# Kernel tuning notes

Hardware: AMD Instinct MI355X
Metric: run time of the kernel (lower is better)

The kernel has to match this reference:

```python
import jax, jax.numpy as jnp
import numpy as np

EPS = 1e-7  # keras backend epsilon
B, D_IN, H, L, DEPTH = 16384, 784, 512, 32, 2

def _lrelu(x):
    return jax.nn.leaky_relu(x, 0.3)  # tf.keras LeakyReLU default alpha

def _router(h, W1, b1, W2, b2, W3, b3):
    h = _lrelu(h @ W1 + b1)
    h = _lrelu(h @ W2 + b2)
    return jax.nn.sigmoid((h @ W3 + b3)[:, 0])

def setup_inputs():
    key = jax.random.key(0)
    ks = jax.random.split(key, 20)
    s = 0.02
    n = lambda k, sh: jax.random.normal(k, sh, jnp.float32) * s
    return {
        'x': jax.random.uniform(ks[0], (B, D_IN), jnp.float32),
        'enc_W0': n(ks[1], (D_IN, H)), 'enc_b0': jnp.zeros((H,), jnp.float32),
        'enc_W': n(ks[2], (3, H, H)), 'enc_b': jnp.zeros((3, H), jnp.float32),
        'dense_Wmu': n(ks[3], (7, H, L)), 'dense_bmu': jnp.zeros((7, L), jnp.float32),
        'dense_Wsig': n(ks[4], (7, H, L)), 'dense_bsig': jnp.zeros((7, L), jnp.float32),
        'trans_Wh': n(ks[5], (6, L, H)), 'trans_bh': jnp.zeros((6, H), jnp.float32),
        'trans_Wmu': n(ks[6], (6, H, L)), 'trans_bmu': jnp.zeros((6, L), jnp.float32),
        'trans_Wsig': n(ks[7], (6, H, L)), 'trans_bsig': jnp.zeros((6, L), jnp.float32),
        'routp_W1': n(ks[8], (3, L, H)), 'routp_b1': jnp.zeros((3, H), jnp.float32),
        'routp_W2': n(ks[9], (3, H, H)), 'routp_b2': jnp.zeros((3, H), jnp.float32),
        'routp_W3': n(ks[10], (3, H, 1)), 'routp_b3': jnp.zeros((3, 1), jnp.float32),
        'routq_W1': n(ks[11], (3, H, H)), 'routq_b1': jnp.zeros((3, H), jnp.float32),
        'routq_W2': n(ks[12], (3, H, H)), 'routq_b2': jnp.zeros((3, H), jnp.float32),
        'routq_W3': n(ks[13], (3, H, 1)), 'routq_b3': jnp.zeros((3, 1), jnp.float32),
        'dec_W1': n(ks[14], (4, L, H)), 'dec_b1': jnp.zeros((4, H), jnp.float32),
        'dec_W2': n(ks[15], (4, H, D_IN)), 'dec_b2': jnp.zeros((4, D_IN), jnp.float32),
    }

def reference(x, enc_W0, enc_b0, enc_W, enc_b,
              dense_Wmu, dense_bmu, dense_Wsig, dense_bsig,
              trans_Wh, trans_bh, trans_Wmu, trans_bmu, trans_Wsig, trans_bsig,
              routp_W1, routp_b1, routp_W2, routp_b2, routp_W3, routp_b3,
              routq_W1, routq_b1, routq_W2, routq_b2, routq_W3, routq_b3,
              dec_W1, dec_b1, dec_W2, dec_b2):
    Bn = x.shape[0]
    # bottom-up encoder chain; encoders collects layers i >= len - (depth+1) = 1
    d = _lrelu(x @ enc_W0 + enc_b0)
    encoders = []
    for i in range(3):
        d = _lrelu(d @ enc_W[i] + enc_b[i])
        encoders.append(d)
    depth_of = [0, 1, 1, 2, 2, 2, 2]  # BFS depth of the 7 tree nodes
    probs = {0: jnp.ones((Bn,), x.dtype)}
    zs = {}
    kl_nodes_tot = jnp.zeros((Bn,), x.dtype)
    kl_dec_tot = jnp.zeros((Bn,), x.dtype)
    kl_root = None
    leaves_prob, recons = [], []
    base = jax.random.key(1)
    for k in range(7):
        dl = depth_of[k]
        d = encoders[DEPTH - dl]
        mu_q_hat = d @ dense_Wmu[k] + dense_bmu[k]
        sig_q_hat = jax.nn.softplus(d @ dense_Wsig[k] + dense_bsig[k])
        if k == 0:
            mu_p = jnp.zeros_like(mu_q_hat)
            sig_p = jnp.ones_like(sig_q_hat)
            mu_q, sig_q = mu_q_hat, sig_q_hat
        else:
            zp = zs[(k - 1) // 2]
            h = _lrelu(zp @ trans_Wh[k - 1] + trans_bh[k - 1])
            mu_p = h @ trans_Wmu[k - 1] + trans_bmu[k - 1]
            sig_p = jax.nn.softplus(h @ trans_Wsig[k - 1] + trans_bsig[k - 1])
            # compute_posterior: precision-weighted fusion
            sig_q = 1.0 / (1.0 / sig_q_hat + 1.0 / sig_p)
            mu_q = sig_q * (mu_q_hat / sig_q_hat + mu_p / sig_p)
        vq = sig_q + EPS
        vp = sig_p + EPS
        # KL(N(mu_q, vq) || N(mu_p, vp)) for diag Gaussians (scale = sqrt(sigma+eps))
        kl = 0.5 * jnp.sum(vq / vp + (mu_q - mu_p) ** 2 / vp - 1.0 + jnp.log(vp / vq), axis=1)
        kl_node = jnp.clip(probs[k] * kl, -1.0, 1000.0)
        if k == 0:
            kl_root = kl_node
        else:
            kl_nodes_tot = kl_nodes_tot + kl_node
        eps_n = jax.random.normal(jax.random.fold_in(base, k), mu_q.shape, x.dtype)
        z = mu_q + jnp.sqrt(vq) * eps_n  # reparameterized sample
        zs[k] = z
        if k < 3:  # internal node: routing
            pl = _router(z, routp_W1[k], routp_b1[k], routp_W2[k], routp_b2[k], routp_W3[k], routp_b3[k])
            plq = _router(d, routq_W1[k], routq_b1[k], routq_W2[k], routq_b2[k], routq_W3[k], routq_b3[k])
            kl_dec = plq * jnp.log(EPS + plq / (pl + EPS)) + (1.0 - plq) * jnp.log(EPS + (1.0 - plq) / (1.0 - pl + EPS))
            kl_dec_tot = kl_dec_tot + probs[k] * kl_dec
            probs[2 * k + 1] = probs[k] * plq
            probs[2 * k + 2] = probs[k] * (1.0 - plq)
        else:  # leaf: decode
            leaves_prob.append(probs[k])
            h = _lrelu(z @ dec_W1[k - 3] + dec_b1[k - 3])
            recons.append(jax.nn.sigmoid(h @ dec_W2[k - 3] + dec_b2[k - 3]))
    rec_losses = jnp.zeros((Bn,), x.dtype)
    for p, r in zip(leaves_prob, recons):
        bce = -jnp.sum(x * jnp.log(r + EPS) + (1.0 - x) * jnp.log(1.0 - r + EPS), axis=1)
        rec_losses = rec_losses + p * bce
    # elbo_samples, per-sample total loss (shape [B])
    return kl_nodes_tot + kl_dec_tot + kl_root + rec_losses
```

## Files before the change

### kernel.cpp

```cpp
#include <hip/hip_runtime.h>
#include <cstdint>
#include <cstddef>

#define B_ROWS 16384
#define DIN 784
#define HD 512
#define LD 32
#define BMT 64

typedef __attribute__((ext_vector_type(8))) short short8;
typedef __attribute__((ext_vector_type(4))) float f32x4;
typedef __attribute__((ext_vector_type(4))) unsigned short us4;

struct I4 { int x, y, z, w; };
__device__ inline int i4get(I4 v, int z) { return z == 0 ? v.x : z == 1 ? v.y : z == 2 ? v.z : v.w; }

__device__ inline unsigned short f2bf(float v) {
  union { float f; unsigned u; } x; x.f = v;
  unsigned r = x.u + 0x7fffu + ((x.u >> 16) & 1u);
  return (unsigned short)(r >> 16);
}
__device__ inline float bf2f(unsigned short b) {
  union { unsigned u; float f; } x; x.u = ((unsigned)b) << 16;
  return x.f;
}

__host__ __device__ inline void threefry2x32(uint32_t k0, uint32_t k1,
                                             uint32_t x0, uint32_t x1,
                                             uint32_t& o0, uint32_t& o1) {
  uint32_t ks2 = k0 ^ k1 ^ 0x1BD11BDAu;
#define TF_ROT(x, d) (((x) << (d)) | ((x) >> (32 - (d))))
#define TF_R(r) { x0 += x1; x1 = TF_ROT(x1, r); x1 ^= x0; }
  x0 += k0; x1 += k1;
  TF_R(13) TF_R(15) TF_R(26) TF_R(6)
  x0 += k1; x1 += ks2 + 1u;
  TF_R(17) TF_R(29) TF_R(16) TF_R(24)
  x0 += ks2; x1 += k0 + 2u;
  TF_R(13) TF_R(15) TF_R(26) TF_R(6)
  x0 += k0; x1 += k1 + 3u;
  TF_R(17) TF_R(29) TF_R(16) TF_R(24)
  x0 += k1; x1 += ks2 + 4u;
  TF_R(13) TF_R(15) TF_R(26) TF_R(6)
  x0 += ks2; x1 += k0 + 5u;
  o0 = x0; o1 = x1;
#undef TF_R
#undef TF_ROT
}

__device__ inline float erfinv_f(float x) {
  float w = -log1pf(-x * x);
  float p;
  if (w < 5.0f) {
    w -= 2.5f;
    p = 2.81022636e-08f;
    p = fmaf(p, w, 3.43273939e-07f);
    p = fmaf(p, w, -3.5233877e-06f);
    p = fmaf(p, w, -4.39150654e-06f);
    p = fmaf(p, w, 0.00021858087f);
    p = fmaf(p, w, -0.00125372503f);
    p = fmaf(p, w, -0.00417768164f);
    p = fmaf(p, w, 0.246640727f);
    p = fmaf(p, w, 1.50140941f);
  } else {
    w = sqrtf(w) - 3.0f;
    p = -0.000200214257f;
    p = fmaf(p, w, 0.000100950558f);
    p = fmaf(p, w, 0.00134934322f);
    p = fmaf(p, w, -0.00367342844f);
    p = fmaf(p, w, 0.00573950773f);
    p = fmaf(p, w, -0.0076224613f);
    p = fmaf(p, w, 0.00943887047f);
    p = fmaf(p, w, 1.00167406f);
    p = fmaf(p, w, 2.83297682f);
  }
  return p * x;
}

__device__ inline float jax_normal_elem(uint32_t ka, uint32_t kb, uint32_t idx) {
  uint32_t b1, b2;
  threefry2x32(ka, kb, 0u, idx, b1, b2);
  uint32_t bits = b1 ^ b2;
  uint32_t fb = (bits >> 9) | 0x3f800000u;
  float f = __uint_as_float(fb) - 1.0f;
  const float lo = -0.99999994f;
  float u = f * 2.0f + lo;
  u = fmaxf(u, lo);
  return 1.41421356f * erfinv_f(u);
}

struct WJob {
  unsigned short pi;
  unsigned src_off, dst_off, start;
  short K, N, Np, Kp;
};
struct WJobs { WJob j[56]; unsigned total; };

constexpr WJobs make_jobs() {
  WJobs W{};
  int idx = 0; unsigned start = 0; unsigned d = 0;
  auto add = [&](int pi, unsigned so, int K, int N, int Np, int Kp, unsigned doff) {
    W.j[idx].pi = (unsigned short)pi; W.j[idx].src_off = so; W.j[idx].dst_off = doff;
    W.j[idx].start = start; W.j[idx].K = (short)K; W.j[idx].N = (short)N;
    W.j[idx].Np = (short)Np; W.j[idx].Kp = (short)Kp;
    start += (unsigned)(Np * Kp); ++idx;
  };
  add(0, 0, 784, 512, 512, 832, d); d += 512 * 832;
  for (int i = 0; i < 3; ++i) { add(1, i * 262144u, 512, 512, 512, 512, d); d += 262144; }
  for (int k = 0; k < 7; ++k) { add(2, k * 16384u, 512, 32, 32, 512, d);
                                add(3, k * 16384u, 512, 32, 32, 512, d + 16384); d += 32768; }
  for (int i = 0; i < 6; ++i) { add(4, i * 16384u, 32, 512, 512, 32, d); d += 16384; }
  for (int i = 0; i < 6; ++i) { add(5, i * 16384u, 512, 32, 32, 512, d);
                                add(6, i * 16384u, 512, 32, 32, 512, d + 16384); d += 32768; }
  for (int k = 0; k < 3; ++k) { add(7, k * 16384u, 32, 512, 512, 32, d); d += 16384; }
  for (int k = 0; k < 3; ++k) { add(8, k * 262144u, 512, 512, 512, 512, d); d += 262144; }
  for (int k = 0; k < 3; ++k) { add(9, k * 262144u, 512, 512, 512, 512, d); d += 262144; }
  for (int k = 0; k < 3; ++k) { add(10, k * 262144u, 512, 512, 512, 512, d); d += 262144; }
  for (int i = 0; i < 4; ++i) { add(11, i * 16384u, 32, 512, 512, 32, d); d += 16384; }
  for (int i = 0; i < 4; ++i) { add(12, i * 401408u, 512, 784, 896, 512, d); d += 458752; }
  W.total = start;
  return W;
}
__device__ constexpr WJobs g_jobs = make_jobs();

struct TileTable { unsigned ts[57]; };
constexpr TileTable make_tiles() {
  TileTable T{}; WJobs J = make_jobs();
  unsigned acc = 0;
  for (int i = 0; i < 56; ++i) {
    T.ts[i] = acc;
    acc += (unsigned)(J.j[i].Np / 32) * (unsigned)(J.j[i].Kp / 32);
  }
  T.ts[56] = acc;
  return T;
}
__device__ constexpr TileTable g_tiles = make_tiles();

#define OFF_ENC0T 0u
#define OFF_ENCT 425984u
#define OFF_DENSE 1212416u
#define OFF_TWH 1441792u
#define OFF_TMS 1540096u
#define OFF_RP1 1736704u
#define OFF_RP2 1785856u
#define OFF_RQ1 2572288u
#define OFF_RQ2 3358720u
#define OFF_DC1 4145152u
#define OFF_DC2 4210688u
#define ARENA_ELEMS 6045696u

struct WSrcs { const float* p[13]; };

__global__ void wconv_k(WSrcs srcs, unsigned short* __restrict__ arena) {
  __shared__ unsigned short tile[32][34];
  unsigned bid = blockIdx.x;
  int jo = 0;
#pragma unroll 1
  while (jo + 1 < 56 && g_tiles.ts[jo + 1] <= bid) ++jo;
  const WJob J = g_jobs.j[jo];
  unsigned t = bid - g_tiles.ts[jo];
  unsigned ktiles = (unsigned)J.Kp / 32u;
  unsigned n0 = (t / ktiles) * 32u, k0 = (t % ktiles) * 32u;
  int ty = threadIdx.x >> 3, tx4 = (threadIdx.x & 7) * 4;
  float v0 = 0, v1 = 0, v2 = 0, v3 = 0;
  int kk = (int)k0 + ty;
  if (kk < J.K) {
    const float* sp = srcs.p[J.pi] + J.src_off + (size_t)kk * J.N + n0 + tx4;
    int nb = (int)(n0 + tx4);
    if (nb + 3 < J.N) {
      float4 v = *reinterpret_cast<const float4*>(sp);
      v0 = v.x; v1 = v.y; v2 = v.z; v3 = v.w;
    } else {
      if (nb + 0 < J.N) v0 = sp[0];
      if (nb + 1 < J.N) v1 = sp[1];
      if (nb + 2 < J.N) v2 = sp[2];
      if (nb + 3 < J.N) v3 = sp[3];
    }
  }
  tile[tx4 + 0][ty] = f2bf(v0);
  tile[tx4 + 1][ty] = f2bf(v1);
  tile[tx4 + 2][ty] = f2bf(v2);
  tile[tx4 + 3][ty] = f2bf(v3);
  __syncthreads();
  us4 w;
  w.x = tile[ty][tx4 + 0]; w.y = tile[ty][tx4 + 1];
  w.z = tile[ty][tx4 + 2]; w.w = tile[ty][tx4 + 3];
  *reinterpret_cast<us4*>(&arena[J.dst_off + (size_t)(n0 + ty) * J.Kp + k0 + tx4]) = w;
}

__global__ void xconv_k(const float* __restrict__ x, unsigned short* __restrict__ xb832,
                        unsigned short* __restrict__ xb784) {
  unsigned g = blockIdx.x * 256u + threadIdx.x;
  unsigned r = g / 208u, c4 = g % 208u;
  unsigned c = c4 * 4u;
  float v0 = 0, v1 = 0, v2 = 0, v3 = 0;
  if (c + 3 < 784u) {
    float4 v = *reinterpret_cast<const float4*>(x + (size_t)r * 784u + c);
    v0 = v.x; v1 = v.y; v2 = v.z; v3 = v.w;
  } else {
    if (c + 0 < 784u) v0 = x[(size_t)r * 784u + c + 0];
    if (c + 1 < 784u) v1 = x[(size_t)r * 784u + c + 1];
    if (c + 2 < 784u) v2 = x[(size_t)r * 784u + c + 2];
    if (c + 3 < 784u) v3 = x[(size_t)r * 784u + c + 3];
  }
  us4 w; w.x = f2bf(v0); w.y = f2bf(v1); w.z = f2bf(v2); w.w = f2bf(v3);
  *reinterpret_cast<us4*>(&xb832[(size_t)r * 832u + c]) = w;
  if (c + 3 < 784u)
    *reinterpret_cast<us4*>(&xb784[(size_t)r * 784u + c]) = w;
}

template <int BM, int BN, int BK, int ACT, typename OT>
__global__ void mgemm_k(const unsigned short* __restrict__ A, int sA,
                        const unsigned short* __restrict__ Wt,
                        const float* __restrict__ b1, const float* __restrict__ b2,
                        OT* __restrict__ C, int sC, int Nreal, int K,
                        I4 zAo, I4 zWo, I4 zCo, int zB1, int zB2,
                        const unsigned short* __restrict__ xx) {
  constexpr int WN = BN / 2;
  constexpr int NF = WN / 16;
  constexpr int MR = BM / 32;
  constexpr int KS = BK / 32;
  constexpr int LPR = BK / 8;
  constexpr int RPC = 64 / LPR;
  __shared__ unsigned short As[BM][BK];
  __shared__ unsigned short Bs[BN][BK];
  __shared__ float sums[BM][2];

  int bx, by, bz;
  {
    const int nx = gridDim.x, ny = gridDim.y;
    const int L = blockIdx.x + nx * (blockIdx.y + ny * blockIdx.z);
    const int xw = nx >> 3;
    const int xcd = L & 7, i = L >> 3;
    bx = xcd * xw + i % xw;
    const int rest = i / xw;
    by = rest % ny;
    bz = rest / ny;
  }

  A += i4get(zAo, bz);
  Wt += i4get(zWo, bz);
  C += i4get(zCo, bz);
  b1 += (size_t)bz * zB1;
  if (ACT == 3 || ACT == 4) { if (b2) b2 += (size_t)bz * zB2; }

  const int tid = threadIdx.x;
  const int lane = tid & 63;
  const int wid = tid >> 6;
  const int wr = wid >> 1, wc = wid & 1;
  const int bm = bx * BM;
  const int bn = by * BN;
  const int lr = lane / LPR;
  const int lk = (lane % LPR) * 8;

  f32x4 acc[MR][NF];
#pragma unroll
  for (int m = 0; m < MR; ++m)
#pragma unroll
    for (int n = 0; n < NF; ++n) acc[m][n] = (f32x4){0.f, 0.f, 0.f, 0.f};

  const int ar = wr * (BM / 2) + (lane & 15);
  const int ac = (lane >> 4) * 8;
  const int br = wc * WN + (lane & 15);

  for (int k0 = 0; k0 < K; k0 += BK) {
    constexpr int CA = BM / RPC;
#pragma unroll
    for (int cc = 0; cc < CA / 4; ++cc) {
      int c = wid * (CA / 4) + cc;
      const unsigned short* g = A + (size_t)(bm + c * RPC + lr) * sA + k0 + lk;
      __builtin_amdgcn_global_load_lds(
          (const __attribute__((address_space(1))) void*)g,
          (__attribute__((address_space(3))) void*)(&As[c * RPC][0]), 16, 0, 0);
    }
    constexpr int CB = BN / RPC;
#pragma unroll
    for (int cc = 0; cc < CB / 4; ++cc) {
      int c = wid * (CB / 4) + cc;
      const unsigned short* g = Wt + (size_t)(bn + c * RPC + lr) * K + k0 + lk;
      __builtin_amdgcn_global_load_lds(
          (const __attribute__((address_space(1))) void*)g,
          (__attribute__((address_space(3))) void*)(&Bs[c * RPC][0]), 16, 0, 0);
    }
    __syncthreads();

    short8 aF[MR][KS], bF[NF][KS];
#pragma unroll
    for (int m = 0; m < MR; ++m)
#pragma unroll
      for (int kk = 0; kk < KS; ++kk)
        aF[m][kk] = *reinterpret_cast<const short8*>(&As[ar + m * 16][ac + kk * 32]);
#pragma unroll
    for (int n = 0; n < NF; ++n)
#pragma unroll
      for (int kk = 0; kk < KS; ++kk)
        bF[n][kk] = *reinterpret_cast<const short8*>(&Bs[br + n * 16][ac + kk * 32]);
#pragma unroll
    for (int kk = 0; kk < KS; ++kk)
#pragma unroll
      for (int m = 0; m < MR; ++m)
#pragma unroll
        for (int n = 0; n < NF; ++n)
          acc[m][n] = __builtin_amdgcn_mfma_f32_16x16x32_bf16(aF[m][kk], bF[n][kk], acc[m][n], 0, 0, 0);
    __syncthreads();
  }

  if constexpr (ACT == 4 || ACT == 5) {
    const int row0 = bm + wr * (BM / 2) + (lane >> 4) * 4;
#pragma unroll
    for (int m = 0; m < MR; ++m) {
#pragma unroll
      for (int r = 0; r < 4; ++r) {
        float s = 0.0f;
        int grow = row0 + m * 16 + r;
#pragma unroll
        for (int n = 0; n < NF; ++n) {
          int col = bn + wc * WN + n * 16 + (lane & 15);
          float v = acc[m][n][r];
          if constexpr (ACT == 4) {
            v += b1[col];
            v = (v >= 0.0f) ? v : 0.3f * v;
            s += v * b2[col];
          } else {
            if (col < Nreal) {
              v += b1[col];
              float sp = fmaxf(v, 0.0f) + __logf(1.0f + __expf(-fabsf(v)));
              float xv = bf2f(xx[(size_t)grow * Nreal + col]);
              s += fmaf(xv, v, -sp);
            }
          }
        }
#pragma unroll
        for (int msk = 1; msk < 16; msk <<= 1) s += __shfl_xor(s, msk, 64);
        if ((lane & 15) == 0) sums[wr * (BM / 2) + m * 16 + (lane >> 4) * 4 + r][wc] = s;
      }
    }
    __syncthreads();
    if (tid < BM) {
      float* Cf = (float*)C;
      Cf[(size_t)(bm + tid) * sC + by] = sums[tid][0] + sums[tid][1];
    }
  } else {
#pragma unroll
    for (int m = 0; m < MR; ++m) {
      int row = bm + wr * (BM / 2) + m * 16 + (lane >> 4) * 4;
#pragma unroll
      for (int n = 0; n < NF; ++n) {
        int col = bn + wc * WN + n * 16 + (lane & 15);
        if (col < Nreal) {
#pragma unroll
          for (int r = 0; r < 4; ++r) {
            float v = acc[m][n][r];
            if constexpr (ACT == 3) {
              int nl = col >> 6, cin = col & 63;
              if (cin < 32) {
                v += b1[nl * 32 + cin];
              } else {
                v += b2[nl * 32 + (cin - 32)];
                v = fmaxf(v, 0.0f) + log1pf(__expf(-fabsf(v)));
              }
            } else {
              v += b1[col];
              if (ACT == 1) v = (v >= 0.0f) ? v : 0.3f * v;
            }
            size_t oidx = (size_t)(row + r) * sC + col;
            if constexpr (sizeof(OT) == 2) C[oidx] = (OT)f2bf(v);
            else C[oidx] = (OT)v;
          }
        }
      }
    }
  }
}

struct Keys { uint32_t a[7]; uint32_t b[7]; };

__global__ void node_k(int kstart, Keys keys,
                       const float* __restrict__ musigAll,
                       const float* __restrict__ mupsigAll,
                       const float* __restrict__ probs,
                       unsigned short* __restrict__ zbuf,
                       float* __restrict__ contrib) {
  const int knode = kstart + blockIdx.y;
  const int row = blockIdx.x * 8 + (threadIdx.x >> 5);
  const int j = threadIdx.x & 31;
  const float* mq = musigAll + (size_t)row * 448 + 64 * knode;
  float mqh = mq[j], sqh = mq[32 + j];
  float mu_q, sig_q, mu_p, sig_p;
  if (knode == 0) {
    mu_p = 0.0f; sig_p = 1.0f; mu_q = mqh; sig_q = sqh;
  } else {
    const float* mp = mupsigAll + (size_t)row * 448 + 64 * knode;
    mu_p = mp[j]; sig_p = mp[32 + j];
    sig_q = 1.0f / (1.0f / sqh + 1.0f / sig_p);
    mu_q = sig_q * (mqh / sqh + mu_p / sig_p);
  }
  float vq = sig_q + 1e-7f, vp = sig_p + 1e-7f;
  float dm = mu_q - mu_p;
  float kj = vq / vp + dm * dm / vp - 1.0f + logf(vp / vq);
#pragma unroll
  for (int msk = 1; msk < 32; msk <<= 1) kj += __shfl_xor(kj, msk, 64);
  float e = jax_normal_elem(keys.a[knode], keys.b[knode], (uint32_t)(row * 32 + j));
  zbuf[(size_t)knode * B_ROWS * 32 + (size_t)row * 32 + j] = f2bf(mu_q + sqrtf(vq) * e);
  if (j == 0) {
    float p = (knode == 0) ? 1.0f : probs[(size_t)knode * B_ROWS + row];
    float kn = fminf(fmaxf(p * 0.5f * kj, -1.0f), 1000.0f);
    contrib[(size_t)knode * B_ROWS + row] = kn;
  }
}

__global__ void route_k(int kstart, const float* __restrict__ plp,
                        const float* __restrict__ plqp,
                        const float* __restrict__ rpb3, const float* __restrict__ rqb3,
                        float* __restrict__ probs, float* __restrict__ contrib) {
  const int k = kstart + blockIdx.y;
  const int row = blockIdx.x * 256 + threadIdx.x;
  const float* pp = plp + ((size_t)k * B_ROWS + row) * 4;
  const float* pq = plqp + ((size_t)k * B_ROWS + row) * 4;
  float sl = pp[0] + pp[1] + pp[2] + pp[3];
  float sq = pq[0] + pq[1] + pq[2] + pq[3];
  float pl = 1.0f / (1.0f + expf(-(sl + rpb3[k])));
  float plq = 1.0f / (1.0f + expf(-(sq + rqb3[k])));
  float p = (k == 0) ? 1.0f : probs[(size_t)k * B_ROWS + row];
  float kld = plq * logf(1e-7f + plq / (pl + 1e-7f)) +
              (1.0f - plq) * logf(1e-7f + (1.0f - plq) / (1.0f - pl + 1e-7f));
  contrib[(size_t)(7 + k) * B_ROWS + row] = p * kld;
  probs[(size_t)(2 * k + 1) * B_ROWS + row] = p * plq;
  probs[(size_t)(2 * k + 2) * B_ROWS + row] = p * (1.0f - plq);
}

__global__ void final_k(const float* __restrict__ contrib, const float* __restrict__ probs,
                        const float* __restrict__ pbce, float* __restrict__ out) {
  const int row = blockIdx.x * 256 + threadIdx.x;
  float s = 0.0f;
#pragma unroll
  for (int i = 0; i < 10; ++i) s += contrib[(size_t)i * B_ROWS + row];
#pragma unroll
  for (int l = 0; l < 4; ++l) {
    const float* pb = pbce + ((size_t)l * B_ROWS + row) * 7;
    float bs = 0.0f;
#pragma unroll
    for (int y = 0; y < 7; ++y) bs += pb[y];
    s += probs[(size_t)(3 + l) * B_ROWS + row] * (-bs);
  }
  out[row] = s;
}

extern "C" void kernel_launch(void* const* d_in, const int* in_sizes, int n_in,
                              void* d_out, int out_size, void* d_ws, size_t ws_size,
                              hipStream_t stream) {
  const float* x      = (const float*)d_in[0];
  const float* enc_W0 = (const float*)d_in[1];
  const float* enc_b0 = (const float*)d_in[2];
  const float* enc_W  = (const float*)d_in[3];
  const float* enc_b  = (const float*)d_in[4];
  const float* dWmu   = (const float*)d_in[5];
  const float* dbmu   = (const float*)d_in[6];
  const float* dWsig  = (const float*)d_in[7];
  const float* dbsig  = (const float*)d_in[8];
  const float* tWh    = (const float*)d_in[9];
  const float* tbh    = (const float*)d_in[10];
  const float* tWmu   = (const float*)d_in[11];
  const float* tbmu   = (const float*)d_in[12];
  const float* tWsig  = (const float*)d_in[13];
  const float* tbsig  = (const float*)d_in[14];
  const float* rpW1   = (const float*)d_in[15];
  const float* rpb1   = (const float*)d_in[16];
  const float* rpW2   = (const float*)d_in[17];
  const float* rpb2   = (const float*)d_in[18];
  const float* rpW3   = (const float*)d_in[19];
  const float* rpb3   = (const float*)d_in[20];
  const float* rqW1   = (const float*)d_in[21];
  const float* rqb1   = (const float*)d_in[22];
  const float* rqW2   = (const float*)d_in[23];
  const float* rqb2   = (const float*)d_in[24];
  const float* rqW3   = (const float*)d_in[25];
  const float* rqb3   = (const float*)d_in[26];
  const float* dcW1   = (const float*)d_in[27];
  const float* dcb1   = (const float*)d_in[28];
  const float* dcW2   = (const float*)d_in[29];
  const float* dcb2   = (const float*)d_in[30];
  float* out = (float*)d_out;
  (void)in_sizes; (void)n_in; (void)out_size; (void)ws_size;

  const size_t BR = B_ROWS;
  unsigned short* h = (unsigned short*)d_ws;
  unsigned short* encA  = h;
  unsigned short* encB  = h + BR * 512;
  unsigned short* encC  = h + BR * 1024;
  unsigned short* bufT  = h + BR * 1536;
  unsigned short* zbuf  = h + BR * 2560;
  unsigned short* xb784 = h + BR * 2784;
  unsigned short* arena = h + BR * 3568;
  size_t ho = BR * 3568 + ARENA_ELEMS;
  float* f = (float*)(h + ho);
  float* musigAll  = f;
  float* mupsigAll = f + BR * 448;
  float* probs     = f + BR * 896;
  float* plp       = f + BR * 903;
  float* plqp      = f + BR * 915;
  float* pbce      = f + BR * 927;
  float* contrib   = f + BR * 955;
  unsigned short* xb832 = (unsigned short*)f;

  const int offA = 0;
  const int offC = (int)(BR * 1024);
  const int offT = (int)(BR * 1536);

  Keys keys;
  for (int k = 0; k < 7; ++k) threefry2x32(0u, 1u, 0u, (uint32_t)k, keys.a[k], keys.b[k]);

  const I4 Z0 = {0, 0, 0, 0};
  constexpr TileTable HT = make_tiles();

  xconv_k<<<dim3((B_ROWS * 208) / 256), 256, 0, stream>>>(x, xb832, xb784);
  WSrcs srcs;
  srcs.p[0] = enc_W0; srcs.p[1] = enc_W; srcs.p[2] = dWmu; srcs.p[3] = dWsig;
  srcs.p[4] = tWh; srcs.p[5] = tWmu; srcs.p[6] = tWsig;
  srcs.p[7] = rpW1; srcs.p[8] = rpW2; srcs.p[9] = rqW1; srcs.p[10] = rqW2;
  srcs.p[11] = dcW1; srcs.p[12] = dcW2;
  wconv_k<<<dim3(HT.ts[56]), 256, 0, stream>>>(srcs, arena);

#define LAUNCH(BN, BK, ACT, OT, A, sA, W, B1, B2, Cc, sC, Nr, K, gy, gz, zA, zW, zC, zb1, zb2, XX) \
  mgemm_k<BMT, BN, BK, ACT, OT><<<dim3(B_ROWS / BMT, gy, gz), 256, 0, stream>>>( \
      A, sA, W, B1, B2, Cc, sC, Nr, K, zA, zW, zC, zb1, zb2, XX)

  LAUNCH(128, 32, 1, unsigned short, xb832, 832, arena + OFF_ENC0T, enc_b0, nullptr,
         bufT, 512, 512, 832, 4, 1, Z0, Z0, Z0, 0, 0, nullptr);
  LAUNCH(128, 32, 1, unsigned short, bufT, 512, arena + OFF_ENCT + 0u, enc_b + 0, nullptr,
         encA, 512, 512, 512, 4, 1, Z0, Z0, Z0, 0, 0, nullptr);
  LAUNCH(128, 32, 3, float, encA, 512, arena + OFF_DENSE + 3u * 32768u, dbmu + 96, dbsig + 96,
         musigAll + 192, 448, 256, 512, 2, 1, Z0, Z0, Z0, 0, 0, nullptr);
  LAUNCH(128, 32, 1, unsigned short, encA, 512, arena + OFF_ENCT + 262144u, enc_b + 512, nullptr,
         encB, 512, 512, 512, 4, 1, Z0, Z0, Z0, 0, 0, nullptr);
  LAUNCH(128, 32, 3, float, encB, 512, arena + OFF_DENSE + 32768u, dbmu + 32, dbsig + 32,
         musigAll + 64, 448, 128, 512, 1, 1, Z0, Z0, Z0, 0, 0, nullptr);
  LAUNCH(128, 32, 1, unsigned short, encB, 512, arena + OFF_ENCT + 524288u, enc_b + 1024, nullptr,
         encC, 512, 512, 512, 4, 1, Z0, Z0, Z0, 0, 0, nullptr);
  LAUNCH(64, 32, 3, float, encC, 512, arena + OFF_DENSE, dbmu, dbsig,
         musigAll, 448, 64, 512, 1, 1, Z0, Z0, Z0, 0, 0, nullptr);
  LAUNCH(128, 32, 1, unsigned short, encC, 512, arena + OFF_RQ1, rqb1, nullptr,
         bufT, 512, 512, 512, 4, 1, Z0, Z0, Z0, 0, 0, nullptr);
  {
    I4 zW = {0, 262144, 0, 0}, zC = {offA, offC, 0, 0};
    LAUNCH(128, 32, 1, unsigned short, encB, 512, arena + OFF_RQ1 + 262144u, rqb1 + 512, nullptr,
           h, 512, 512, 512, 4, 2, Z0, zW, zC, 512, 0, nullptr);
  }
  {
    I4 zA = {offT, offA, offC, 0};
    I4 zW = {0, 262144, 524288, 0};
    I4 zC = {0, (int)(BR * 4), (int)(BR * 8), 0};
    LAUNCH(128, 32, 4, float, h, 512, arena + OFF_RQ2, rqb2, rqW3,
           plqp, 4, 512, 512, 4, 3, zA, zW, zC, 512, 512, nullptr);
  }

  node_k<<<dim3(B_ROWS / 8, 1), 256, 0, stream>>>(0, keys, musigAll, mupsigAll, probs, zbuf, contrib);
  LAUNCH(128, 32, 1, unsigned short, zbuf, 32, arena + OFF_RP1, rpb1, nullptr,
         bufT, 512, 512, 32, 4, 1, Z0, Z0, Z0, 0, 0, nullptr);
  LAUNCH(128, 32, 4, float, bufT, 512, arena + OFF_RP2, rpb2, rpW3,
         plp, 4, 512, 512, 4, 1, Z0, Z0, Z0, 0, 0, nullptr);
  route_k<<<dim3(B_ROWS / 256, 1), 256, 0, stream>>>(0, plp, plqp, rpb3, rqb3, probs, contrib);

  LAUNCH(128, 32, 1, unsigned short, zbuf, 32, arena + OFF_TWH, tbh, nullptr,
         bufT, 1024, 1024, 32, 8, 1, Z0, Z0, Z0, 0, 0, nullptr);
  {
    I4 zA = {0, 512, 0, 0}, zW = {0, 32768, 0, 0}, zC = {0, 64, 0, 0};
    LAUNCH(64, 32, 3, float, bufT, 1024, arena + OFF_TMS, tbmu, tbsig,
           mupsigAll + 64, 448, 64, 512, 1, 2, zA, zW, zC, 32, 32, nullptr);
  }
  node_k<<<dim3(B_ROWS / 8, 2), 256, 0, stream>>>(1, keys, musigAll, mupsigAll, probs, zbuf, contrib);
  {
    I4 zA = {0, (int)(BR * 32), 0, 0}, zW = {0, 16384, 0, 0}, zC = {offA, offC, 0, 0};
    LAUNCH(128, 32, 1, unsigned short, zbuf + BR * 32, 32, arena + OFF_RP1 + 16384u, rpb1 + 512, nullptr,
           h, 512, 512, 32, 4, 2, zA, zW, zC, 512, 0, nullptr);
    I4 zA2 = {offA, offC, 0, 0}, zW2 = {0, 262144, 0, 0}, zC2 = {0, (int)(BR * 4), 0, 0};
    LAUNCH(128, 32, 4, float, h, 512, arena + OFF_RP2 + 262144u, rpb2 + 512, rpW3 + 512,
           plp + BR * 4, 4, 512, 512, 4, 2, zA2, zW2, zC2, 512, 512, nullptr);
  }
  route_k<<<dim3(B_ROWS / 256, 2), 256, 0, stream>>>(1, plp, plqp, rpb3, rqb3, probs, contrib);

  {
    I4 zA = {0, (int)(BR * 32), 0, 0};
    I4 zW = {0, 32768, 0, 0};
    I4 zC = {0, (int)(BR * 1024), 0, 0};
    LAUNCH(128, 32, 1, unsigned short, zbuf + BR * 32, 32, arena + OFF_TWH + 32768u, tbh + 1024, nullptr,
           h, 1024, 1024, 32, 8, 2, zA, zW, zC, 1024, 0, nullptr);
    I4 zA2 = {0, 512, (int)(BR * 1024), (int)(BR * 1024 + 512)};
    I4 zW2 = {0, 32768, 65536, 98304};
    I4 zC2 = {0, 64, 128, 192};
    LAUNCH(64, 32, 3, float, h, 1024, arena + OFF_TMS + 65536u, tbmu + 64, tbsig + 64,
           mupsigAll + 192, 448, 64, 512, 1, 4, zA2, zW2, zC2, 32, 32, nullptr);
  }
  node_k<<<dim3(B_ROWS / 8, 4), 256, 0, stream>>>(3, keys, musigAll, mupsigAll, probs, zbuf, contrib);

  {
    I4 zA1 = {0, (int)(BR * 32), (int)(BR * 64), (int)(BR * 96)};
    I4 zW1 = {0, 16384, 32768, 49152};
    I4 zC1 = {0, (int)(BR * 512), (int)(BR * 1024), (int)(BR * 1536)};
    LAUNCH(128, 32, 1, unsigned short, zbuf + BR * 96, 32, arena + OFF_DC1, dcb1, nullptr,
           h, 512, 512, 32, 4, 4, zA1, zW1, zC1, 512, 0, nullptr);
    I4 zA2 = {0, (int)(BR * 512), (int)(BR * 1024), (int)(BR * 1536)};
    I4 zW2 = {0, 458752, 917504, 1376256};
    I4 zC2 = {0, (int)(BR * 7), (int)(BR * 14), (int)(BR * 21)};
    mgemm_k<128, 128, 32, 5, float><<<dim3(B_ROWS / 128, 7, 4), 256, 0, stream>>>(
        h, 512, arena + OFF_DC2, dcb2, nullptr,
        pbce, 7, 784, 512, zA2, zW2, zC2, 784, 0, xb784);
  }

  final_k<<<dim3(B_ROWS / 256), 256, 0, stream>>>(contrib, probs, pbce, out);
#undef LAUNCH
}
```

Baseline: 613.0 us.

## Add double-buffered 8-wave GEMM variant for large-K bf16 layers

Generalises the MFMA GEMM kernel over wave count and LDS buffer depth. A DB=2 path prefetches the next K tile via global_load_lds while the current one is computed, using explicit vmcnt waits and barriers. The big K=512/832 GEMMs now launch with 512-thread, 128-row blocks. This aims to hide global-load latency and raise per-block reuse, at the cost of more LDS per block and possibly lower occupancy.

Measured after the change: 567.0 us. 7.5% less time.

```diff
diff --git a/kernel.cpp b/kernel.cpp
--- a/kernel.cpp
+++ b/kernel.cpp
@@ -6,7 +6,6 @@
 #define DIN 784
 #define HD 512
 #define LD 32
-#define BMT 64
 
 typedef __attribute__((ext_vector_type(8))) short short8;
 typedef __attribute__((ext_vector_type(4))) float f32x4;
@@ -208,22 +207,28 @@
     *reinterpret_cast<us4*>(&xb784[(size_t)r * 784u + c]) = w;
 }
 
-template <int BM, int BN, int BK, int ACT, typename OT>
-__global__ void mgemm_k(const unsigned short* __restrict__ A, int sA,
-                        const unsigned short* __restrict__ Wt,
-                        const float* __restrict__ b1, const float* __restrict__ b2,
-                        OT* __restrict__ C, int sC, int Nreal, int K,
-                        I4 zAo, I4 zWo, I4 zCo, int zB1, int zB2,
-                        const unsigned short* __restrict__ xx) {
-  constexpr int WN = BN / 2;
+template <int BM, int BN, int BK, int NW, int DB, int ACT, typename OT>
+__global__ __launch_bounds__(NW * 64)
+void mgemm_k(const unsigned short* __restrict__ A, int sA,
+             const unsigned short* __restrict__ Wt,
+             const float* __restrict__ b1, const float* __restrict__ b2,
+             OT* __restrict__ C, int sC, int Nreal, int K,
+             I4 zAo, I4 zWo, I4 zCo, int zB1, int zB2,
+             const unsigned short* __restrict__ xx) {
+  constexpr int WCN = NW / 2;
+  constexpr int WN = BN / WCN;
   constexpr int NF = WN / 16;
-  constexpr int MR = BM / 32;
+  constexpr int MR = BM / 2 / 16;
   constexpr int KS = BK / 32;
   constexpr int LPR = BK / 8;
   constexpr int RPC = 64 / LPR;
-  __shared__ unsigned short As[BM][BK];
-  __shared__ unsigned short Bs[BN][BK];
-  __shared__ float sums[BM][2];
+  constexpr int CA = BM / RPC, CB = BN / RPC;
+  constexpr int CAW = (CA >= NW) ? CA / NW : 1;
+  constexpr int CBW = (CB >= NW) ? CB / NW : 1;
+  constexpr int LPW = CAW + CBW;
+  __shared__ unsigned short As[DB][BM][BK];
+  __shared__ unsigned short Bs[DB][BN][BK];
+  __shared__ float sums[BM][WCN];
 
   int bx, by, bz;
   {
@@ -246,12 +251,35 @@
   const int tid = threadIdx.x;
   const int lane = tid & 63;
   const int wid = tid >> 6;
-  const int wr = wid >> 1, wc = wid & 1;
+  const int wr = wid / WCN, wc = wid % WCN;
   const int bm = bx * BM;
   const int bn = by * BN;
   const int lr = lane / LPR;
   const int lk = (lane % LPR) * 8;
 
+  auto stage = [&](int buf, int k0) {
+#pragma unroll
+    for (int cc = 0; cc < CAW; ++cc) {
+      int c = wid * CAW + cc;
+      if (CAW * NW == CA || c < CA) {
+        const unsigned short* g = A + (size_t)(bm + c * RPC + lr) * sA + k0 + lk;
+        __builtin_amdgcn_global_load_lds(
+            (const __attribute__((address_space(1))) void*)g,
+            (__attribute__((address_space(3))) void*)(&As[buf][c * RPC][0]), 16, 0, 0);
+      }
+    }
+#pragma unroll
+    for (int cc = 0; cc < CBW; ++cc) {
+      int c = wid * CBW + cc;
+      if (CBW * NW == CB || c < CB) {
+        const unsigned short* g = Wt + (size_t)(bn + c * RPC + lr) * K + k0 + lk;
+        __builtin_amdgcn_global_load_lds(
+            (const __attribute__((address_space(1))) void*)g,
+            (__attribute__((address_space(3))) void*)(&Bs[buf][c * RPC][0]), 16, 0, 0);
+      }
+    }
+  };
+
   f32x4 acc[MR][NF];
 #pragma unroll
   for (int m = 0; m < MR; ++m)
@@ -261,39 +289,20 @@
   const int ar = wr * (BM / 2) + (lane & 15);
   const int ac = (lane >> 4) * 8;
   const int br = wc * WN + (lane & 15);
-
-  for (int k0 = 0; k0 < K; k0 += BK) {
-    constexpr int CA = BM / RPC;
-#pragma unroll
-    for (int cc = 0; cc < CA / 4; ++cc) {
-      int c = wid * (CA / 4) + cc;
-      const unsigned short* g = A + (size_t)(bm + c * RPC + lr) * sA + k0 + lk;
-      __builtin_amdgcn_global_load_lds(
-          (const __attribute__((address_space(1))) void*)g,
-          (__attribute__((address_space(3))) void*)(&As[c * RPC][0]), 16, 0, 0);
-    }
-    constexpr int CB = BN / RPC;
-#pragma unroll
-    for (int cc = 0; cc < CB / 4; ++cc) {
-      int c = wid * (CB / 4) + cc;
-      const unsigned short* g = Wt + (size_t)(bn + c * RPC + lr) * K + k0 + lk;
-      __builtin_amdgcn_global_load_lds(
-          (const __attribute__((address_space(1))) void*)g,
-          (__attribute__((address_space(3))) void*)(&Bs[c * RPC][0]), 16, 0, 0);
-    }
-    __syncthreads();
-
+  const int nt = K / BK;
+
+  auto compute = [&](int buf) {
     short8 aF[MR][KS], bF[NF][KS];
 #pragma unroll
     for (int m = 0; m < MR; ++m)
 #pragma unroll
       for (int kk = 0; kk < KS; ++kk)
-        aF[m][kk] = *reinterpret_cast<const short8*>(&As[ar + m * 16][ac + kk * 32]);
+        aF[m][kk] = *reinterpret_cast<const short8*>(&As[buf][ar + m * 16][ac + kk * 32]);
 #pragma unroll
     for (int n = 0; n < NF; ++n)
 #pragma unroll
       for (int kk = 0; kk < KS; ++kk)
-        bF[n][kk] = *reinterpret_cast<const short8*>(&Bs[br + n * 16][ac + kk * 32]);
+        bF[n][kk] = *reinterpret_cast<const short8*>(&Bs[buf][br + n * 16][ac + kk * 32]);
 #pragma unroll
     for (int kk = 0; kk < KS; ++kk)
 #pragma unroll
@@ -301,7 +310,33 @@
 #pragma unroll
         for (int n = 0; n < NF; ++n)
           acc[m][n] = __builtin_amdgcn_mfma_f32_16x16x32_bf16(aF[m][kk], bF[n][kk], acc[m][n], 0, 0, 0);
-    __syncthreads();
+  };
+
+  if constexpr (DB == 2) {
+    stage(0, 0);
+    for (int t = 0; t < nt; ++t) {
+      if (t + 1 < nt) {
+        stage((t + 1) & 1, (t + 1) * BK);
+        if constexpr (LPW == 2) asm volatile("s_waitcnt vmcnt(2)" ::: "memory");
+        else if constexpr (LPW == 3) asm volatile("s_waitcnt vmcnt(3)" ::: "memory");
+        else asm volatile("s_waitcnt vmcnt(4)" ::: "memory");
+      } else {
+        asm volatile("s_waitcnt vmcnt(0)" ::: "memory");
+      }
+      __builtin_amdgcn_s_barrier();
+      asm volatile("" ::: "memory");
+      compute(t & 1);
+      asm volatile("" ::: "memory");
+      __builtin_amdgcn_s_barrier();
+      asm volatile("" ::: "memory");
+    }
+  } else {
+    for (int t = 0; t < nt; ++t) {
+      stage(0, t * BK);
+      __syncthreads();
+      compute(0);
+      __syncthreads();
+    }
   }
 
   if constexpr (ACT == 4 || ACT == 5) {
@@ -336,8 +371,11 @@
     }
     __syncthreads();
     if (tid < BM) {
+      float t = 0.0f;
+#pragma unroll
+      for (int wv = 0; wv < WCN; ++wv) t += sums[tid][wv];
       float* Cf = (float*)C;
-      Cf[(size_t)(bm + tid) * sC + by] = sums[tid][0] + sums[tid][1];
+      Cf[(size_t)(bm + tid) * sC + by] = t;
     }
   } else {
 #pragma unroll
@@ -521,43 +559,46 @@
   wconv_k<<<dim3(HT.ts[56]), 256, 0, stream>>>(srcs, arena);
 
 #define LAUNCH(BN, BK, ACT, OT, A, sA, W, B1, B2, Cc, sC, Nr, K, gy, gz, zA, zW, zC, zb1, zb2, XX) \
-  mgemm_k<BMT, BN, BK, ACT, OT><<<dim3(B_ROWS / BMT, gy, gz), 256, 0, stream>>>( \
+  mgemm_k<64, BN, BK, 4, 1, ACT, OT><<<dim3(B_ROWS / 64, gy, gz), 256, 0, stream>>>( \
       A, sA, W, B1, B2, Cc, sC, Nr, K, zA, zW, zC, zb1, zb2, XX)
-
-  LAUNCH(128, 32, 1, unsigned short, xb832, 832, arena + OFF_ENC0T, enc_b0, nullptr,
-         bufT, 512, 512, 832, 4, 1, Z0, Z0, Z0, 0, 0, nullptr);
-  LAUNCH(128, 32, 1, unsigned short, bufT, 512, arena + OFF_ENCT + 0u, enc_b + 0, nullptr,
-         encA, 512, 512, 512, 4, 1, Z0, Z0, Z0, 0, 0, nullptr);
+#define LAUNCH8(BN, BK, ACT, OT, A, sA, W, B1, B2, Cc, sC, Nr, K, gy, gz, zA, zW, zC, zb1, zb2, XX) \
+  mgemm_k<128, BN, BK, 8, 2, ACT, OT><<<dim3(B_ROWS / 128, gy, gz), 512, 0, stream>>>( \
+      A, sA, W, B1, B2, Cc, sC, Nr, K, zA, zW, zC, zb1, zb2, XX)
+
+  LAUNCH8(128, 32, 1, unsigned short, xb832, 832, arena + OFF_ENC0T, enc_b0, nullptr,
+          bufT, 512, 512, 832, 4, 1, Z0, Z0, Z0, 0, 0, nullptr);
+  LAUNCH8(128, 32, 1, unsigned short, bufT, 512, arena + OFF_ENCT + 0u, enc_b + 0, nullptr,
+          encA, 512, 512, 512, 4, 1, Z0, Z0, Z0, 0, 0, nullptr);
   LAUNCH(128, 32, 3, float, encA, 512, arena + OFF_DENSE + 3u * 32768u, dbmu + 96, dbsig + 96,
          musigAll + 192, 448, 256, 512, 2, 1, Z0, Z0, Z0, 0, 0, nullptr);
-  LAUNCH(128, 32, 1, unsigned short, encA, 512, arena + OFF_ENCT + 262144u, enc_b + 512, nullptr,
-         encB, 512, 512, 512, 4, 1, Z0, Z0, Z0, 0, 0, nullptr);
+  LAUNCH8(128, 32, 1, unsigned short, encA, 512, arena + OFF_ENCT + 262144u, enc_b + 512, nullptr,
+          encB, 512, 512, 512, 4, 1, Z0, Z0, Z0, 0, 0, nullptr);
   LAUNCH(128, 32, 3, float, encB, 512, arena + OFF_DENSE + 32768u, dbmu + 32, dbsig + 32,
          musigAll + 64, 448, 128, 512, 1, 1, Z0, Z0, Z0, 0, 0, nullptr);
-  LAUNCH(128, 32, 1, unsigned short, encB, 512, arena + OFF_ENCT + 524288u, enc_b + 1024, nullptr,
-         encC, 512, 512, 512, 4, 1, Z0, Z0, Z0, 0, 0, nullptr);
+  LAUNCH8(128, 32, 1, unsigned short, encB, 512, arena + OFF_ENCT + 524288u, enc_b + 1024, nullptr,
+          encC, 512, 512, 512, 4, 1, Z0, Z0, Z0, 0, 0, nullptr);
   LAUNCH(64, 32, 3, float, encC, 512, arena + OFF_DENSE, dbmu, dbsig,
          musigAll, 448, 64, 512, 1, 1, Z0, Z0, Z0, 0, 0, nullptr);
-  LAUNCH(128, 32, 1, unsigned short, encC, 512, arena + OFF_RQ1, rqb1, nullptr,
-         bufT, 512, 512, 512, 4, 1, Z0, Z0, Z0, 0, 0, nullptr);
+  LAUNCH8(128, 32, 1, unsigned short, encC, 512, arena + OFF_RQ1, rqb1, nullptr,
+          bufT, 512, 512, 512, 4, 1, Z0, Z0, Z0, 0, 0, nullptr);
   {
     I4 zW = {0, 262144, 0, 0}, zC = {offA, offC, 0, 0};
-    LAUNCH(128, 32, 1, unsigned short, encB, 512, arena + OFF_RQ1 + 262144u, rqb1 + 512, nullptr,
-           h, 512, 512, 512, 4, 2, Z0, zW, zC, 512, 0, nullptr);
+    LAUNCH8(128, 32, 1, unsigned short, encB, 512, arena + OFF_RQ1 + 262144u, rqb1 + 512, nullptr,
+            h, 512, 512, 512, 4, 2, Z0, zW, zC, 512, 0, nullptr);
   }
   {
     I4 zA = {offT, offA, offC, 0};
     I4 zW = {0, 262144, 524288, 0};
     I4 zC = {0, (int)(BR * 4), (int)(BR * 8), 0};
-    LAUNCH(128, 32, 4, float, h, 512, arena + OFF_RQ2, rqb2, rqW3,
-           plqp, 4, 512, 512, 4, 3, zA, zW, zC, 512, 512, nullptr);
+    LAUNCH8(128, 32, 4, float, h, 512, arena + OFF_RQ2, rqb2, rqW3,
+            plqp, 4, 512, 512, 4, 3, zA, zW, zC, 512, 512, nullptr);
   }
 
   node_k<<<dim3(B_ROWS / 8, 1), 256, 0, stream>>>(0, keys, musigAll, mupsigAll, probs, zbuf, contrib);
   LAUNCH(128, 32, 1, unsigned short, zbuf, 32, arena + OFF_RP1, rpb1, nullptr,
          bufT, 512, 512, 32, 4, 1, Z0, Z0, Z0, 0, 0, nullptr);
-  LAUNCH(128, 32, 4, float, bufT, 512, arena + OFF_RP2, rpb2, rpW3,
-         plp, 4, 512, 512, 4, 1, Z0, Z0, Z0, 0, 0, nullptr);
+  LAUNCH8(128, 32, 4, float, bufT, 512, arena + OFF_RP2, rpb2, rpW3,
+          plp, 4, 512, 512, 4, 1, Z0, Z0, Z0, 0, 0, nullptr);
   route_k<<<dim3(B_ROWS / 256, 1), 256, 0, stream>>>(0, plp, plqp, rpb3, rqb3, probs, contrib);
 
   LAUNCH(128, 32, 1, unsigned short, zbuf, 32, arena + OFF_TWH, tbh, nullptr,
@@ -573,8 +614,8 @@
     LAUNCH(128, 32, 1, unsigned short, zbuf + BR * 32, 32, arena + OFF_RP1 + 16384u, rpb1 + 512, nullptr,
            h, 512, 512, 32, 4, 2, zA, zW, zC, 512, 0, nullptr);
     I4 zA2 = {offA, offC, 0, 0}, zW2 = {0, 262144, 0, 0}, zC2 = {0, (int)(BR * 4), 0, 0};
-    LAUNCH(128, 32, 4, float, h, 512, arena + OFF_RP2 + 262144u, rpb2 + 512, rpW3 + 512,
-           plp + BR * 4, 4, 512, 512, 4, 2, zA2, zW2, zC2, 512, 512, nullptr);
+    LAUNCH8(128, 32, 4, float, h, 512, arena + OFF_RP2 + 262144u, rpb2 + 512, rpW3 + 512,
+            plp + BR * 4, 4, 512, 512, 4, 2, zA2, zW2, zC2, 512, 512, nullptr);
   }
   route_k<<<dim3(B_ROWS / 256, 2), 256, 0, stream>>>(1, plp, plqp, rpb3, rqb3, probs, contrib);
 
@@ -601,11 +642,11 @@
     I4 zA2 = {0, (int)(BR * 512), (int)(BR * 1024), (int)(BR * 1536)};
     I4 zW2 = {0, 458752, 917504, 1376256};
     I4 zC2 = {0, (int)(BR * 7), (int)(BR * 14), (int)(BR * 21)};
-    mgemm_k<128, 128, 32, 5, float><<<dim3(B_ROWS / 128, 7, 4), 256, 0, stream>>>(
-        h, 512, arena + OFF_DC2, dcb2, nullptr,
-        pbce, 7, 784, 512, zA2, zW2, zC2, 784, 0, xb784);
+    LAUNCH8(128, 32, 5, float, h, 512, arena + OFF_DC2, dcb2, nullptr,
+            pbce, 7, 784, 512, 7, 4, zA2, zW2, zC2, 784, 0, xb784);
   }
 
   final_k<<<dim3(B_ROWS / 256), 256, 0, stream>>>(contrib, probs, pbce, out);
 #undef LAUNCH
-}
+#undef LAUNCH8
+}
```
